# Kernel optimization log

Measured on AMD Instinct MI355X. Metric: run time of the kernel, lower is better.

Reference implementation:

```python
import jax, jax.numpy as jnp
import numpy as np

HIDDEN = 768
OUT_DIM = 128
IN_DIM = OUT_DIM + 1  # LSTM input_size = output_dim + 1
T, B = 512, 256


def setup_inputs() -> dict:
    key = jax.random.key(0)
    ks = jax.random.split(key, 8)
    s = 1.0 / np.sqrt(HIDDEN)  # torch LSTM/Linear init scale
    seq = jax.random.normal(ks[0], (T, B, IN_DIM), dtype=jnp.float32)
    W_ih = jax.random.uniform(ks[1], (4 * HIDDEN, IN_DIM), minval=-s, maxval=s, dtype=jnp.float32)
    W_hh = jax.random.uniform(ks[2], (4 * HIDDEN, HIDDEN), minval=-s, maxval=s, dtype=jnp.float32)
    b_ih = jax.random.uniform(ks[3], (4 * HIDDEN,), minval=-s, maxval=s, dtype=jnp.float32)
    b_hh = jax.random.uniform(ks[4], (4 * HIDDEN,), minval=-s, maxval=s, dtype=jnp.float32)
    W_dec = jax.random.uniform(ks[5], (OUT_DIM, HIDDEN), minval=-s, maxval=s, dtype=jnp.float32)
    b_dec = jax.random.uniform(ks[6], (OUT_DIM,), minval=-s, maxval=s, dtype=jnp.float32)
    return {"sequence": seq, "W_ih": W_ih, "W_hh": W_hh, "b_ih": b_ih,
            "b_hh": b_hh, "W_dec": W_dec, "b_dec": b_dec}


def _lstm(sequence, W_ih, W_hh, b_ih, b_hh):
    # Pre-compute input projections for all timesteps in one big GEMM: [T,B,4H]
    x_proj = jnp.einsum('tbd,gd->tbg', sequence, W_ih) + (b_ih + b_hh)
    H = W_hh.shape[1]

    def step(carry, xp_t):
        h, c = carry
        gates = xp_t + h @ W_hh.T                      # [B,4H]
        i, f, g, o = jnp.split(gates, 4, axis=-1)      # torch gate order i,f,g,o
        i = jax.nn.sigmoid(i)
        f = jax.nn.sigmoid(f)
        g = jnp.tanh(g)
        o = jax.nn.sigmoid(o)
        c = f * c + i * g
        h = o * jnp.tanh(c)
        return (h, c), h

    Bsz = sequence.shape[1]
    h0 = jnp.zeros((Bsz, H), dtype=sequence.dtype)
    c0 = jnp.zeros((Bsz, H), dtype=sequence.dtype)
    (h_t, c_t), hidden_seq = jax.lax.scan(step, (h0, c0), x_proj)
    return hidden_seq, h_t, c_t


def reference(sequence, W_ih, W_hh, b_ih, b_hh, W_dec, b_dec):
    length = sequence.shape[0] // 2
    hidden_seq, h_t, c_t = _lstm(sequence, W_ih, W_hh, b_ih, b_hh)
    # decode the second (readout) half of the sequence; dropout is identity in eval
    out = jnp.einsum('tbh,oh->tbo', hidden_seq[length:], W_dec) + b_dec
    return out
```

## Files before the change

kernel.cpp:

```cpp
#include <hip/hip_runtime.h>
#include <cstdint>
#include <cstddef>

#define TT 512
#define BB 256
#define HID 768
#define INDIM 129
#define INPAD 160
#define OUTD 128
#define KS_TOT 58
#define KS_REC 48
#define XSTR 168
#define GSTR 100

typedef __attribute__((ext_vector_type(8))) short bf16x8;
typedef __attribute__((ext_vector_type(4))) float f32x4;
typedef __attribute__((ext_vector_type(16))) float f32x16;
typedef unsigned short u16;
typedef unsigned long long u64;

#define MFMA32(A, B, C) __builtin_amdgcn_mfma_f32_32x32x16_bf16(A, B, C, 0, 0, 0)
#define ZERO16 {0.f,0.f,0.f,0.f,0.f,0.f,0.f,0.f,0.f,0.f,0.f,0.f,0.f,0.f,0.f,0.f}

__device__ __forceinline__ u16 f2bf(float f) {
  union { float f; unsigned u; } v; v.f = f;
  unsigned u = v.u;
  u += 0x7fffu + ((u >> 16) & 1u);
  return (u16)(u >> 16);
}
__device__ __forceinline__ float sigm(float x) { return 1.0f / (1.0f + __expf(-x)); }
__device__ __forceinline__ float tanh_fast(float x) { return 2.0f / (1.0f + __expf(-2.0f * x)) - 1.0f; }

__global__ __launch_bounds__(256) void prep_kernel(
    const float* __restrict__ W_ih, const float* __restrict__ W_hh,
    const float* __restrict__ b_ih, const float* __restrict__ b_hh,
    const float* __restrict__ W_dec, const float* __restrict__ b_dec,
    u16* __restrict__ Wpack, u16* __restrict__ Wdpack,
    float* __restrict__ biasg, u16* __restrict__ h0,
    unsigned* __restrict__ flags, float* __restrict__ out) {
  const int stride = blockDim.x * gridDim.x;
  const int i0 = blockIdx.x * blockDim.x + threadIdx.x;

  for (int i = i0; i < 32 * 3 * KS_TOT * 512; i += stride) {
    int jj = i & 7, lane = (i >> 3) & 63, r = i >> 9;
    int ks = r % KS_TOT; int r2 = r / KS_TOT;
    int nt = r2 % 3, ct = r2 / 3;
    int p = nt * 32 + (lane & 31);
    int g = p / 24, j = p - g * 24;
    int row = g * HID + ct * 24 + j;
    int kh = (lane >> 5) * 8 + jj;
    float v;
    if (ks < KS_REC) v = W_hh[(size_t)row * HID + ks * 16 + kh];
    else { int d = (ks - KS_REC) * 16 + kh; v = (d < INDIM) ? W_ih[(size_t)row * INDIM + d] : 0.f; }
    Wpack[i] = f2bf(v);
  }
  for (int i = i0; i < 4 * 48 * 512; i += stride) {
    int jj = i & 7, lane = (i >> 3) & 63, r = i >> 9;
    int ks = r % 48, nt = r / 48;
    int orow = nt * 32 + (lane & 31);
    int k = ks * 16 + (lane >> 5) * 8 + jj;
    Wdpack[i] = f2bf(W_dec[(size_t)orow * HID + k]);
  }
  for (int i = i0; i < 4 * HID; i += stride) biasg[i] = b_ih[i] + b_hh[i];
  for (int i = i0; i < BB * HID; i += stride) h0[i] = (u16)0;
  for (int i = i0; i < 256; i += stride) flags[i] = 0u;
  for (int i = i0; i < 256 * BB * OUTD; i += stride) out[i] = b_dec[i & (OUTD - 1)];
}

__device__ __forceinline__ void waitflags(unsigned* fl, unsigned target, int lane) {
  for (;;) {
    unsigned v = __hip_atomic_load(&fl[lane & 31], __ATOMIC_RELAXED, __HIP_MEMORY_SCOPE_AGENT);
    if (__all((int)(v >= target))) break;
    __builtin_amdgcn_s_sleep(1);
  }
}
__device__ __forceinline__ void waitflags8(unsigned* fl8, unsigned target, int lane) {
  for (;;) {
    unsigned v = __hip_atomic_load(&fl8[lane & 7], __ATOMIC_RELAXED, __HIP_MEMORY_SCOPE_AGENT);
    if (__all((int)(v >= target))) break;
    __builtin_amdgcn_s_sleep(1);
  }
}

#define HLOAD(i, off) asm volatile( \
    "global_load_dwordx4 %0, %1, off offset:" #off " sc0 sc1" \
    : "=v"(hreg[i]) : "v"(hrow) : "memory")
#define VMWAIT(n) do { asm volatile("s_waitcnt vmcnt(" #n ")" ::: "memory"); \
    __builtin_amdgcn_sched_barrier(0); } while (0)

__global__ __launch_bounds__(256, 1) void lstm_persist(
    const float* __restrict__ seq, const u16* __restrict__ Wpack,
    const u16* __restrict__ Wdpack, const float* __restrict__ biasg,
    u16* __restrict__ hb0, u16* __restrict__ hb1,
    unsigned* __restrict__ flags, float* __restrict__ out) {
  __shared__ float gbuf[4][32 * GSTR];
  __shared__ u16 xlds[32 * XSTR];
  __shared__ float biasl[96];

  const int tid = threadIdx.x;
  const int w = tid >> 6;
  const int lane = tid & 63;
  const int l5 = lane & 31;
  const int hi = lane >> 5;
  const int bid = blockIdx.x;
  const int bt = bid >> 5;
  const int ct = bid & 31;
  const int b0 = bt * 32;
  unsigned* fl = flags + bt * 32;

  for (int i = tid; i < 32 * 31; i += 256) {
    int r = i / 31, d = INDIM + i - r * 31;
    xlds[r * XSTR + d] = (u16)0;
  }
  if (tid < 96) biasl[tid] = biasg[(tid / 24) * HID + ct * 24 + (tid % 24)];

  bf16x8 Breg[3][12];
  #pragma unroll
  for (int t = 0; t < 12; ++t)
    #pragma unroll
    for (int nt = 0; nt < 3; ++nt)
      Breg[nt][t] = *(const bf16x8*)(Wpack +
          (((size_t)(ct * 3 + nt)) * KS_TOT + (w * 12 + t)) * 512 + (size_t)lane * 8);

  const int icnt = (w < 2) ? 3 : 2;
  const int ioff = (w <= 2) ? w * 3 : 8;
  bf16x8 Bireg[3][3] = {};
  #pragma unroll
  for (int u = 0; u < 3; ++u)
    if (u < icnt) {
      #pragma unroll
      for (int nt = 0; nt < 3; ++nt)
        Bireg[u][nt] = *(const bf16x8*)(Wpack +
            (((size_t)(ct * 3 + nt)) * KS_TOT + KS_REC + ioff + u) * 512 + (size_t)lane * 8);
    }

  {
    const float* xs = seq + (size_t)b0 * INDIM;
    for (int i = tid; i < 32 * INDIM; i += 256) {
      int r = i / INDIM, d = i - r * INDIM;
      xlds[r * XSTR + d] = f2bf(xs[i]);
    }
  }

  float creg[4] = {0.f, 0.f, 0.f, 0.f};
  const int cr = tid / 6, cg = tid - (tid / 6) * 6;
  __syncthreads();

  for (int s = 0; s < TT; ++s) {
    const u16* hbprev = (s & 1) ? hb1 : hb0;
    u16* hbnext       = (s & 1) ? hb0 : hb1;

    f32x16 acc[3] = {ZERO16, ZERO16, ZERO16};
    #pragma unroll
    for (int u = 0; u < 3; ++u)
      if (u < icnt) {
        int kk = ioff + u;
        bf16x8 a = *(const bf16x8*)(xlds + l5 * XSTR + kk * 16 + hi * 8);
        acc[0] = MFMA32(a, Bireg[u][0], acc[0]);
        acc[1] = MFMA32(a, Bireg[u][1], acc[1]);
        acc[2] = MFMA32(a, Bireg[u][2], acc[2]);
      }

    waitflags8(fl + 8 * w, (unsigned)s, lane);

    bf16x8 hreg[12];
    {
      const u64 hrow = (u64)(hbprev + (size_t)(b0 + l5) * HID + w * 192 + hi * 8);
      HLOAD(0, 0);   HLOAD(1, 32);  HLOAD(2, 64);  HLOAD(3, 96);
      HLOAD(4, 128); HLOAD(5, 160); HLOAD(6, 192); HLOAD(7, 224);
      HLOAD(8, 256); HLOAD(9, 288); HLOAD(10, 320); HLOAD(11, 352);
    }
    VMWAIT(6);
    #pragma unroll
    for (int t = 0; t < 6; ++t) {
      acc[0] = MFMA32(hreg[t], Breg[0][t], acc[0]);
      acc[1] = MFMA32(hreg[t], Breg[1][t], acc[1]);
      acc[2] = MFMA32(hreg[t], Breg[2][t], acc[2]);
    }
    VMWAIT(0);
    #pragma unroll
    for (int t = 6; t < 12; ++t) {
      acc[0] = MFMA32(hreg[t], Breg[0][t], acc[0]);
      acc[1] = MFMA32(hreg[t], Breg[1][t], acc[1]);
      acc[2] = MFMA32(hreg[t], Breg[2][t], acc[2]);
    }

    {
      float* gb = gbuf[w];
      #pragma unroll
      for (int nt = 0; nt < 3; ++nt)
        #pragma unroll
        for (int r = 0; r < 16; ++r) {
          int row = (r & 3) + 8 * (r >> 2) + 4 * hi;
          gb[row * GSTR + nt * 32 + l5] = acc[nt][r];
        }
    }

    float xf[17];
    if (s + 1 < TT) {
      const float* xs = seq + ((size_t)(s + 1) * BB + b0) * INDIM;
      #pragma unroll
      for (int k = 0; k < 17; ++k) {
        int i = tid + k * 256;
        xf[k] = (i < 32 * INDIM) ? xs[i] : 0.f;
      }
    }
    __syncthreads();

    if (tid < 192) {
      float gv4[4][4];
      #pragma unroll
      for (int g = 0; g < 4; ++g) {
        f32x4 v = *(f32x4*)&gbuf[0][cr * GSTR + g * 24 + cg * 4];
        #pragma unroll
        for (int w2 = 1; w2 < 4; ++w2)
          v += *(f32x4*)&gbuf[w2][cr * GSTR + g * 24 + cg * 4];
        #pragma unroll
        for (int e = 0; e < 4; ++e) gv4[g][e] = v[e] + biasl[g * 24 + cg * 4 + e];
      }
      u64 pack = 0;
      #pragma unroll
      for (int e = 0; e < 4; ++e) {
        float iv = sigm(gv4[0][e]), fv = sigm(gv4[1][e]);
        float gg = tanh_fast(gv4[2][e]), ov = sigm(gv4[3][e]);
        float cn = fv * creg[e] + iv * gg;
        creg[e] = cn;
        pack |= (u64)f2bf(ov * tanh_fast(cn)) << (16 * e);
      }
      __hip_atomic_store((u64*)hbnext + ((size_t)(b0 + cr) * HID + ct * 24 + cg * 4) / 4,
                         pack, __ATOMIC_RELAXED, __HIP_MEMORY_SCOPE_AGENT);
    }
    if (s + 1 < TT) {
      #pragma unroll
      for (int k = 0; k < 17; ++k) {
        int i = tid + k * 256;
        if (i < 32 * INDIM) {
          int r = i / INDIM, d = i - r * INDIM;
          xlds[r * XSTR + d] = f2bf(xf[k]);
        }
      }
    }
    __syncthreads();

    if (tid == 0)
      __hip_atomic_store(&fl[ct], (unsigned)(s + 1), __ATOMIC_RELAXED, __HIP_MEMORY_SCOPE_AGENT);

    if (s >= 257 && ((ct >> 2) == ((s - 257) & 7))) {
      const int ont = ct & 3;
      f32x16 dacc = ZERO16;
      #pragma unroll
      for (int t = 0; t < 12; ++t) {
        int ks = w * 12 + t;
        bf16x8 b = *(const bf16x8*)(Wdpack + (((size_t)ont * 48 + ks) * 64 + lane) * 8);
        dacc = MFMA32(hreg[t], b, dacc);
      }
      float* ob = out + ((size_t)(s - 257) * BB + b0) * OUTD + ont * 32;
      #pragma unroll
      for (int r = 0; r < 16; ++r) {
        int row = (r & 3) + 8 * (r >> 2) + 4 * hi;
        atomicAdd(&ob[(size_t)row * OUTD + l5], dacc[r]);
      }
    }
  }

  if ((ct >> 2) == 7) {
    waitflags(fl, (unsigned)TT, lane);
    const int ont = ct & 3;
    const u64* hq = (const u64*)hb0;
    f32x16 acc = ZERO16;
    #pragma unroll
    for (int t = 0; t < 12; ++t) {
      int ks = w * 12 + t;
      union { u64 q[2]; bf16x8 v; } a;
      size_t base = ((size_t)(b0 + l5) * HID + ks * 16 + hi * 8) / 4;
      a.q[0] = __hip_atomic_load(hq + base,     __ATOMIC_RELAXED, __HIP_MEMORY_SCOPE_AGENT);
      a.q[1] = __hip_atomic_load(hq + base + 1, __ATOMIC_RELAXED, __HIP_MEMORY_SCOPE_AGENT);
      bf16x8 b = *(const bf16x8*)(Wdpack + (((size_t)ont * 48 + ks) * 64 + lane) * 8);
      acc = MFMA32(a.v, b, acc);
    }
    float* ob = out + ((size_t)255 * BB + b0) * OUTD + ont * 32;
    #pragma unroll
    for (int r = 0; r < 16; ++r) {
      int row = (r & 3) + 8 * (r >> 2) + 4 * hi;
      atomicAdd(&ob[(size_t)row * OUTD + l5], acc[r]);
    }
  }
}

extern "C" void kernel_launch(void* const* d_in, const int* in_sizes, int n_in,
                              void* d_out, int out_size, void* d_ws, size_t ws_size,
                              hipStream_t stream) {
  (void)in_sizes; (void)n_in; (void)out_size; (void)ws_size;
  const float* seq   = (const float*)d_in[0];
  const float* W_ih  = (const float*)d_in[1];
  const float* W_hh  = (const float*)d_in[2];
  const float* b_ih  = (const float*)d_in[3];
  const float* b_hh  = (const float*)d_in[4];
  const float* W_dec = (const float*)d_in[5];
  const float* b_dec = (const float*)d_in[6];
  float* out = (float*)d_out;

  u16* Wpack  = (u16*)d_ws;
  u16* Wdpack = Wpack + 32 * 3 * KS_TOT * 512;
  u16* h0     = Wdpack + 4 * 48 * 512;
  u16* h1     = h0 + BB * HID;
  float* biasg = (float*)(h1 + BB * HID);
  unsigned* flags = (unsigned*)(biasg + 4 * HID);

  prep_kernel<<<2048, 256, 0, stream>>>(W_ih, W_hh, b_ih, b_hh, W_dec, b_dec,
                                        Wpack, Wdpack, biasg, h0, flags, out);
  lstm_persist<<<256, 256, 0, stream>>>(seq, Wpack, Wdpack, biasg,
                                        h0, h1, flags, out);
}
```

Measured before the change: 3.199 ms.

## Use per-wave fine-grained step flags and keep decoder weights in registers

Replaces the per-block step flag, which was set after a block-wide barrier, with per-wave flags. Each wave publishes its flag as soon as its own h slice is stored, and consumers poll only the three producer waves that wrote the columns they need. The h loads are now issued right after the poll, before the input-projection MFMAs, and the next-step x loads are moved earlier. Decoder weights are preloaded into registers instead of being re-read from global memory each decode step. The aim is to shorten the critical path of the cross-block recurrence, at the cost of more registers and more flag traffic; correctness depends on the vmcnt wait ordering the h store before the flag store.

```diff
diff --git a/kernel.cpp b/kernel.cpp
--- a/kernel.cpp
+++ b/kernel.cpp
@@ -6,7 +6,6 @@
 #define BB 256
 #define HID 768
 #define INDIM 129
-#define INPAD 160
 #define OUTD 128
 #define KS_TOT 58
 #define KS_REC 48
@@ -63,7 +62,7 @@
   }
   for (int i = i0; i < 4 * HID; i += stride) biasg[i] = b_ih[i] + b_hh[i];
   for (int i = i0; i < BB * HID; i += stride) h0[i] = (u16)0;
-  for (int i = i0; i < 256; i += stride) flags[i] = 0u;
+  for (int i = i0; i < 1280; i += stride) flags[i] = 0u;
   for (int i = i0; i < 256 * BB * OUTD; i += stride) out[i] = b_dec[i & (OUTD - 1)];
 }
 
@@ -74,17 +73,24 @@
     __builtin_amdgcn_s_sleep(1);
   }
 }
-__device__ __forceinline__ void waitflags8(unsigned* fl8, unsigned target, int lane) {
-  for (;;) {
-    unsigned v = __hip_atomic_load(&fl8[lane & 7], __ATOMIC_RELAXED, __HIP_MEMORY_SCOPE_AGENT);
-    if (__all((int)(v >= target))) break;
-    __builtin_amdgcn_s_sleep(1);
-  }
-}
-
-#define HLOAD(i, off) asm volatile( \
+__device__ __forceinline__ unsigned flagld(const unsigned* p) {
+  unsigned v; u64 a = (u64)p;
+  asm volatile("global_load_dword %0, %1, off sc0 sc1\n\ts_waitcnt vmcnt(0)"
+               : "=v"(v) : "v"(a) : "memory");
+  return v;
+}
+__device__ __forceinline__ void stflag(unsigned* p, unsigned v) {
+  u64 a = (u64)p;
+  asm volatile("global_store_dword %0, %1, off sc0 sc1" :: "v"(a), "v"(v) : "memory");
+}
+
+#define HLD(i, off) asm volatile( \
     "global_load_dwordx4 %0, %1, off offset:" #off " sc0 sc1" \
     : "=v"(hreg[i]) : "v"(hrow) : "memory")
+#define HLOADS() do { HLD(0,0); HLD(1,32); HLD(2,64); HLD(3,96); \
+    HLD(4,128); HLD(5,160); HLD(6,192); HLD(7,224); \
+    HLD(8,256); HLD(9,288); HLD(10,320); HLD(11,352); } while (0)
+
 #define VMWAIT(n) do { asm volatile("s_waitcnt vmcnt(" #n ")" ::: "memory"); \
     __builtin_amdgcn_sched_barrier(0); } while (0)
 
@@ -92,7 +98,8 @@
     const float* __restrict__ seq, const u16* __restrict__ Wpack,
     const u16* __restrict__ Wdpack, const float* __restrict__ biasg,
     u16* __restrict__ hb0, u16* __restrict__ hb1,
-    unsigned* __restrict__ flags, float* __restrict__ out) {
+    unsigned* __restrict__ sflags, unsigned* __restrict__ fflags,
+    float* __restrict__ out) {
   __shared__ float gbuf[4][32 * GSTR];
   __shared__ u16 xlds[32 * XSTR];
   __shared__ float biasl[96];
@@ -106,7 +113,8 @@
   const int bt = bid >> 5;
   const int ct = bid & 31;
   const int b0 = bt * 32;
-  unsigned* fl = flags + bt * 32;
+  unsigned* sfl = sflags + bt * 128;
+  unsigned* ffl = fflags + bt * 32;
 
   for (int i = tid; i < 32 * 31; i += 256) {
     int r = i / 31, d = INDIM + i - r * 31;
@@ -134,6 +142,12 @@
             (((size_t)(ct * 3 + nt)) * KS_TOT + KS_REC + ioff + u) * 512 + (size_t)lane * 8);
     }
 
+  bf16x8 Dreg[12];
+  #pragma unroll
+  for (int t = 0; t < 12; ++t)
+    Dreg[t] = *(const bf16x8*)(Wdpack +
+        (((size_t)(ct & 3) * 48 + w * 12 + t) * 64 + lane) * 8);
+
   {
     const float* xs = seq + (size_t)b0 * INDIM;
     for (int i = tid; i < 32 * INDIM; i += 256) {
@@ -144,11 +158,26 @@
 
   float creg[4] = {0.f, 0.f, 0.f, 0.f};
   const int cr = tid / 6, cg = tid - (tid / 6) * 6;
+  const unsigned* sfp = sfl + ((lane < 24) ? ((8 * w + lane / 3) * 4 + (lane % 3))
+                                           : (8 * w) * 4);
+
   __syncthreads();
 
   for (int s = 0; s < TT; ++s) {
     const u16* hbprev = (s & 1) ? hb1 : hb0;
     u16* hbnext       = (s & 1) ? hb0 : hb1;
+
+    for (;;) {
+      unsigned v = flagld(sfp);
+      if (__all((int)(v >= (unsigned)s))) break;
+      __builtin_amdgcn_s_sleep(1);
+    }
+
+    bf16x8 hreg[12];
+    {
+      const u64 hrow = (u64)(hbprev + (size_t)(b0 + l5) * HID + w * 192 + hi * 8);
+      HLOADS();
+    }
 
     f32x16 acc[3] = {ZERO16, ZERO16, ZERO16};
     #pragma unroll
@@ -161,15 +190,6 @@
         acc[2] = MFMA32(a, Bireg[u][2], acc[2]);
       }
 
-    waitflags8(fl + 8 * w, (unsigned)s, lane);
-
-    bf16x8 hreg[12];
-    {
-      const u64 hrow = (u64)(hbprev + (size_t)(b0 + l5) * HID + w * 192 + hi * 8);
-      HLOAD(0, 0);   HLOAD(1, 32);  HLOAD(2, 64);  HLOAD(3, 96);
-      HLOAD(4, 128); HLOAD(5, 160); HLOAD(6, 192); HLOAD(7, 224);
-      HLOAD(8, 256); HLOAD(9, 288); HLOAD(10, 320); HLOAD(11, 352);
-    }
     VMWAIT(6);
     #pragma unroll
     for (int t = 0; t < 6; ++t) {
@@ -185,26 +205,27 @@
       acc[2] = MFMA32(hreg[t], Breg[2][t], acc[2]);
     }
 
+    float xf[17];
+    if (s + 1 < TT) {
+      const float* xs = seq + ((size_t)(s + 1) * BB + b0) * INDIM;
+      #pragma unroll
+      for (int k = 0; k < 17; ++k) {
+        int i = tid + k * 256;
+        xf[k] = (i < 32 * INDIM) ? xs[i] : 0.f;
+      }
+    }
+
     {
-      float* gb = gbuf[w];
+      float* gbw = &gbuf[w][0];
       #pragma unroll
       for (int nt = 0; nt < 3; ++nt)
         #pragma unroll
         for (int r = 0; r < 16; ++r) {
           int row = (r & 3) + 8 * (r >> 2) + 4 * hi;
-          gb[row * GSTR + nt * 32 + l5] = acc[nt][r];
+          gbw[row * GSTR + nt * 32 + l5] = acc[nt][r];
         }
     }
 
-    float xf[17];
-    if (s + 1 < TT) {
-      const float* xs = seq + ((size_t)(s + 1) * BB + b0) * INDIM;
-      #pragma unroll
-      for (int k = 0; k < 17; ++k) {
-        int i = tid + k * 256;
-        xf[k] = (i < 32 * INDIM) ? xs[i] : 0.f;
-      }
-    }
     __syncthreads();
 
     if (tid < 192) {
@@ -221,15 +242,19 @@
       u64 pack = 0;
       #pragma unroll
       for (int e = 0; e < 4; ++e) {
-        float iv = sigm(gv4[0][e]), fv = sigm(gv4[1][e]);
+        float iv = sigm(gv4[0][e]), fv2 = sigm(gv4[1][e]);
         float gg = tanh_fast(gv4[2][e]), ov = sigm(gv4[3][e]);
-        float cn = fv * creg[e] + iv * gg;
+        float cn = fv2 * creg[e] + iv * gg;
         creg[e] = cn;
         pack |= (u64)f2bf(ov * tanh_fast(cn)) << (16 * e);
       }
       __hip_atomic_store((u64*)hbnext + ((size_t)(b0 + cr) * HID + ct * 24 + cg * 4) / 4,
                          pack, __ATOMIC_RELAXED, __HIP_MEMORY_SCOPE_AGENT);
-    }
+      asm volatile("s_waitcnt vmcnt(0)" ::: "memory");
+      __builtin_amdgcn_sched_barrier(0);
+      if (lane == 0) stflag(sfl + ct * 4 + w, (unsigned)(s + 1));
+    }
+
     if (s + 1 < TT) {
       #pragma unroll
       for (int k = 0; k < 17; ++k) {
@@ -240,20 +265,12 @@
         }
       }
     }
-    __syncthreads();
-
-    if (tid == 0)
-      __hip_atomic_store(&fl[ct], (unsigned)(s + 1), __ATOMIC_RELAXED, __HIP_MEMORY_SCOPE_AGENT);
 
     if (s >= 257 && ((ct >> 2) == ((s - 257) & 7))) {
       const int ont = ct & 3;
       f32x16 dacc = ZERO16;
       #pragma unroll
-      for (int t = 0; t < 12; ++t) {
-        int ks = w * 12 + t;
-        bf16x8 b = *(const bf16x8*)(Wdpack + (((size_t)ont * 48 + ks) * 64 + lane) * 8);
-        dacc = MFMA32(hreg[t], b, dacc);
-      }
+      for (int t = 0; t < 12; ++t) dacc = MFMA32(hreg[t], Dreg[t], dacc);
       float* ob = out + ((size_t)(s - 257) * BB + b0) * OUTD + ont * 32;
       #pragma unroll
       for (int r = 0; r < 16; ++r) {
@@ -261,28 +278,29 @@
         atomicAdd(&ob[(size_t)row * OUTD + l5], dacc[r]);
       }
     }
-  }
+
+    __syncthreads();
+  }
+
+  if (tid == 0) stflag(ffl + ct, (unsigned)TT);
 
   if ((ct >> 2) == 7) {
-    waitflags(fl, (unsigned)TT, lane);
+    waitflags(ffl, (unsigned)TT, lane);
     const int ont = ct & 3;
-    const u64* hq = (const u64*)hb0;
-    f32x16 acc = ZERO16;
-    #pragma unroll
-    for (int t = 0; t < 12; ++t) {
-      int ks = w * 12 + t;
-      union { u64 q[2]; bf16x8 v; } a;
-      size_t base = ((size_t)(b0 + l5) * HID + ks * 16 + hi * 8) / 4;
-      a.q[0] = __hip_atomic_load(hq + base,     __ATOMIC_RELAXED, __HIP_MEMORY_SCOPE_AGENT);
-      a.q[1] = __hip_atomic_load(hq + base + 1, __ATOMIC_RELAXED, __HIP_MEMORY_SCOPE_AGENT);
-      bf16x8 b = *(const bf16x8*)(Wdpack + (((size_t)ont * 48 + ks) * 64 + lane) * 8);
-      acc = MFMA32(a.v, b, acc);
-    }
+    bf16x8 hreg[12];
+    {
+      const u64 hrow = (u64)(hb0 + (size_t)(b0 + l5) * HID + w * 192 + hi * 8);
+      HLOADS();
+    }
+    VMWAIT(0);
+    f32x16 dacc = ZERO16;
+    #pragma unroll
+    for (int t = 0; t < 12; ++t) dacc = MFMA32(hreg[t], Dreg[t], dacc);
     float* ob = out + ((size_t)255 * BB + b0) * OUTD + ont * 32;
     #pragma unroll
     for (int r = 0; r < 16; ++r) {
       int row = (r & 3) + 8 * (r >> 2) + 4 * hi;
-      atomicAdd(&ob[(size_t)row * OUTD + l5], acc[r]);
+      atomicAdd(&ob[(size_t)row * OUTD + l5], dacc[r]);
     }
   }
 }
@@ -305,10 +323,11 @@
   u16* h0     = Wdpack + 4 * 48 * 512;
   u16* h1     = h0 + BB * HID;
   float* biasg = (float*)(h1 + BB * HID);
-  unsigned* flags = (unsigned*)(biasg + 4 * HID);
+  unsigned* sflags = (unsigned*)(biasg + 4 * HID);
+  unsigned* fflags = sflags + 1024;
 
   prep_kernel<<<2048, 256, 0, stream>>>(W_ih, W_hh, b_ih, b_hh, W_dec, b_dec,
-                                        Wpack, Wdpack, biasg, h0, flags, out);
+                                        Wpack, Wdpack, biasg, h0, sflags, out);
   lstm_persist<<<256, 256, 0, stream>>>(seq, Wpack, Wdpack, biasg,
-                                        h0, h1, flags, out);
-}
+                                        h0, h1, sflags, fflags, out);
+}
```

Result: faster. 2.884 ms (-9.9%).
